# Performance work log

Hardware: AMD Instinct MI355X
Metric: run time of the kernel (lower is better)

Reference implementation:

```python
import jax, jax.numpy as jnp
import numpy as np

CUTOFF = 5.0
RBF_DIM = 32
CS, CV = 64, 32          # 64x0e + 32x1o -> irreps dim 64 + 32*3 = 160
NODE_ATTR = 64
HID = 128
NBLK = 3
MAXZ = 100
B, N, E = 32, 64, 131072
NW = 2 * CS + 3 * CV     # radial weights: w_ss, w_vv, w_sv, w_vs, w_vx


def setup_inputs() -> dict:
    key = jax.random.key(0)
    ks = jax.random.split(key, 16)
    z = jax.random.randint(ks[0], (B, N), 0, MAXZ + 1)
    mask = jnp.ones((B, N), jnp.float32)
    absorber_index = jax.random.randint(ks[1], (B,), 0, N)
    edge_src = jax.random.randint(ks[2], (E,), 0, B * N)
    edge_dst = jax.random.randint(ks[3], (E,), 0, B * N)
    edge_weight = 0.1 + (CUTOFF - 0.1) * jax.random.uniform(ks[4], (E,))
    edge_vec = jax.random.normal(ks[5], (E, 3))
    s = 0.1
    z_emb = s * jax.random.normal(ks[6], (MAXZ + 1, NODE_ATTR))
    W_in = s * jax.random.normal(ks[7], (NODE_ATTR + 1, CS))
    W1 = s * jax.random.normal(ks[8], (NBLK, RBF_DIM, HID))
    b1 = jnp.zeros((NBLK, HID))
    W2 = s * jax.random.normal(ks[9], (NBLK, HID, NW))
    b2 = jnp.zeros((NBLK, NW))
    Ws = s * jax.random.normal(ks[10], (NBLK, CS + CV, CS))
    Wv = s * jax.random.normal(ks[11], (NBLK, CS + 2 * CV, CV))
    Wg = s * jax.random.normal(ks[12], (NBLK, CS, CV))
    alpha = 0.1 * jnp.ones((NBLK,))
    return dict(z=z, mask=mask, absorber_index=absorber_index, edge_src=edge_src,
                edge_dst=edge_dst, edge_weight=edge_weight, edge_vec=edge_vec,
                z_emb=z_emb, W_in=W_in, W1=W1, b1=b1, W2=W2, b2=b2,
                Ws=Ws, Wv=Wv, Wg=Wg, alpha=alpha)


def _encode(z, mask, absorber_index, edge_src, edge_dst, edge_weight, edge_vec,
            z_emb, W_in, W1, b1, W2, b2, Ws, Wv, Wg, alpha):
    b, n = z.shape
    bn = b * n
    # absorber one-hot flag + atomic-number embedding -> scalar input irreps
    abs_flag = jnp.zeros((b, n), jnp.float32).at[jnp.arange(b), absorber_index].set(1.0)
    zf = z_emb[z]                                               # (B,N,NODE_ATTR)
    scalar_in = jnp.concatenate([zf, abs_flag[..., None]], -1).reshape(bn, NODE_ATTR + 1)
    s = scalar_in @ W_in                                        # (BN,CS)  0e channels
    v = jnp.zeros((bn, CV, 3), s.dtype)                         # 1o channels (o3.Linear from 0e only)
    fm = mask.reshape(bn)
    s = s * fm[:, None]

    # edge features: Gaussian RBF on clamped length + component-normalized SH (l<=1)
    el = edge_weight
    ed = edge_vec / jnp.clip(el, 1e-8)[:, None]
    d = jnp.minimum(el, CUTOFF)
    centers = jnp.linspace(0.0, CUTOFF, RBF_DIM)
    delta = CUTOFF / (RBF_DIM - 1)
    rbf = jnp.exp(-0.5 * ((d[:, None] - centers) / delta) ** 2)  # (E,RBF_DIM)
    Y1 = jnp.sqrt(3.0) * ed                                      # l=1 SH, 'component' norm; Y0 == 1
    env = 0.5 * (jnp.cos(jnp.pi * el / CUTOFF) + 1.0) * (el < CUTOFF)  # cosine cutoff

    sqrt3 = jnp.sqrt(3.0)
    sqrt2 = jnp.sqrt(2.0)
    for i in range(NBLK):
        h = jax.nn.silu(rbf @ W1[i] + b1[i])                     # radial MLP
        w = (h @ W2[i] + b2[i]) * env[:, None]                   # (E,NW) per-edge TP weights
        w_ss, w_vv, w_sv, w_vs, w_vx = jnp.split(
            w, [CS, CS + CV, 2 * CS + CV, 2 * CS + 2 * CV], axis=-1)
        s_src = s[edge_src]                                      # gather (E,CS)
        v_src = v[edge_src]                                      # gather (E,CV,3)
        # depthwise (uvu) tensor-product paths
        m_s = jnp.concatenate([
            w_ss * s_src,                                        # 0e x 0e -> 0e
            w_vv * jnp.einsum('ecd,ed->ec', v_src, Y1) / sqrt3,  # 1o x 1o -> 0e
        ], -1)                                                   # (E,CS+CV)
        m_v = jnp.concatenate([
            w_sv[:, :, None] * s_src[:, :, None] * Y1[:, None, :],           # 0e x 1o -> 1o
            w_vs[:, :, None] * v_src,                                        # 1o x 0e -> 1o
            w_vx[:, :, None] * jnp.cross(v_src, Y1[:, None, :]) / sqrt2,     # 1o x 1o -> 1o
        ], 1)                                                    # (E,CS+2CV,3)
        agg_s = jnp.zeros((bn, CS + CV), s.dtype).at[edge_dst].add(m_s)
        agg_v = jnp.zeros((bn, CS + 2 * CV, 3), s.dtype).at[edge_dst].add(m_v)
        # irreps-wise linear + gated nonlinearity + scaled residual
        us = jax.nn.silu(agg_s @ Ws[i])                          # (BN,CS)
        uv = jnp.einsum('bcd,ce->bed', agg_v, Wv[i])             # (BN,CV,3)
        g = jax.nn.sigmoid(us @ Wg[i])                           # (BN,CV) gates
        uv = uv * g[:, :, None]
        s = s + alpha[i] * us
        v = v + alpha[i] * uv

    # IrrepNorm: RMS-normalize each irrep block over its channels
    eps = 1e-6
    s = s / jnp.sqrt(jnp.mean(s ** 2, -1, keepdims=True) + eps)
    vn = jnp.mean(jnp.sum(v ** 2, -1), -1, keepdims=True)        # (BN,1)
    v = v / jnp.sqrt(vn + eps)[..., None]
    s = s * fm[:, None]
    v = v * fm[:, None, None]
    out = jnp.concatenate([s, v.reshape(bn, CV * 3)], -1)
    return out.reshape(b, n, CS + 3 * CV)


def reference(z, mask, absorber_index, edge_src, edge_dst, edge_weight, edge_vec,
              z_emb, W_in, W1, b1, W2, b2, Ws, Wv, Wg, alpha):
    return _encode(z, mask, absorber_index, edge_src, edge_dst, edge_weight, edge_vec,
                   z_emb, W_in, W1, b1, W2, b2, Ws, Wv, Wg, alpha)
```

## Files before the change

### kernel.cpp

```cpp
#include <hip/hip_runtime.h>

#define CSC 64
#define CVC 32
#define HIDC 128
#define NWC 224
#define RBFD 32
#define CUTF 5.0f

typedef __attribute__((ext_vector_type(8))) short bfrag8;
typedef __attribute__((ext_vector_type(4))) float facc4;

__device__ __forceinline__ unsigned short f2bf(float x) {
    union { float f; unsigned int u; } a; a.f = x;
    unsigned int u = a.u;
    return (unsigned short)((u + 0x7fffu + ((u >> 16) & 1u)) >> 16);
}
__device__ __forceinline__ float bf2f(unsigned int u16) {
    union { float f; unsigned int v; } x; x.v = u16 << 16; return x.f;
}

__device__ __forceinline__ float siluf(float x) { return x / (1.0f + __expf(-x)); }
__device__ __forceinline__ float sigmf(float x) { return 1.0f / (1.0f + __expf(-x)); }

__global__ __launch_bounds__(256) void eae_zero_int(int* __restrict__ p, int n) {
    int i = blockIdx.x * 256 + threadIdx.x;
    if (i < n) p[i] = 0;
}

__global__ __launch_bounds__(256) void eae_hist_kernel(const int* __restrict__ edge_dst,
                                                       int* __restrict__ cnt, int E) {
    int e = blockIdx.x * 256 + threadIdx.x;
    if (e < E) atomicAdd(&cnt[edge_dst[e]], 1);
}

__global__ __launch_bounds__(256) void eae_scan_kernel(const int* __restrict__ cnt,
                                                       int* __restrict__ row_ptr,
                                                       int* __restrict__ cursor, int BN) {
    __shared__ int part[256];
    int t = threadIdx.x;
    int per = (BN + 255) / 256;
    int base = t * per;
    int local[16];
    int lsum = 0;
    for (int i = 0; i < per; ++i) {
        int idx = base + i;
        int c = (idx < BN) ? cnt[idx] : 0;
        local[i] = c; lsum += c;
    }
    part[t] = lsum;
    __syncthreads();
    if (t == 0) {
        int run = 0;
        for (int i = 0; i < 256; ++i) { int v = part[i]; part[i] = run; run += v; }
    }
    __syncthreads();
    int run = part[t];
    for (int i = 0; i < per; ++i) {
        int idx = base + i;
        if (idx < BN) { row_ptr[idx] = run; cursor[idx] = run; run += local[i]; }
    }
    if (t == 255) row_ptr[BN] = run;
}

__global__ __launch_bounds__(256) void eae_scatter_kernel(
    const int* __restrict__ edge_dst, const int* __restrict__ edge_src,
    const float* __restrict__ edge_weight, const float* __restrict__ edge_vec,
    int* __restrict__ cursor, float4* __restrict__ edata, int* __restrict__ esrc,
    unsigned short* __restrict__ rbf_g, int E) {
    int e = blockIdx.x * 256 + threadIdx.x;
    if (e < E) {
        int pos = atomicAdd(&cursor[edge_dst[e]], 1);
        const float SQ3 = 1.7320508075688772f;
        const float PIF = 3.14159265358979323846f;
        const float delta = CUTF / (RBFD - 1);
        const float inv_delta = 1.0f / delta;
        float el = edge_weight[e];
        float inv = 1.0f / fmaxf(el, 1e-8f);
        float4 d;
        d.x = SQ3 * edge_vec[3 * e + 0] * inv;
        d.y = SQ3 * edge_vec[3 * e + 1] * inv;
        d.z = SQ3 * edge_vec[3 * e + 2] * inv;
        d.w = (el < CUTF) ? 0.5f * (__cosf(PIF * el / CUTF) + 1.0f) : 0.0f;
        edata[pos] = d;
        esrc[pos] = edge_src[e];
        float dd = fminf(el, CUTF) * inv_delta;
        unsigned short* rp = rbf_g + (size_t)pos * RBFD;
        #pragma unroll
        for (int k = 0; k < RBFD; ++k) {
            float x = dd - (float)k;
            rp[k] = f2bf(__expf(-0.5f * x * x));
        }
    }
}

__global__ __launch_bounds__(64) void eae_pack_kernel(
    const float* __restrict__ W1, const float* __restrict__ W2,
    unsigned short* __restrict__ W1P, unsigned short* __restrict__ W2P)
{
    int b = blockIdx.x;
    int lane = threadIdx.x;
    int t4 = lane >> 4, lr = lane & 15;
    if (b < 24) {
        int blk = b >> 3, mt = b & 7;
        const float* W1b = W1 + blk * 32 * 128;
        unsigned short* dst = W1P + ((size_t)b * 64 + lane) * 8;
        #pragma unroll
        for (int i = 0; i < 8; ++i) {
            int k = 8 * t4 + i;
            dst[i] = f2bf(W1b[k * HIDC + 16 * mt + lr]);
        }
    } else {
        int idx = b - 24;
        int blk = idx >> 6, rem = idx & 63;
        int mt = rem >> 2, ks = rem & 3;
        const float* W2b = W2 + blk * 128 * 224;
        unsigned short* dst = W2P + ((size_t)idx * 64 + lane) * 8;
        int ch = 16 * mt + lr;
        #pragma unroll
        for (int i = 0; i < 8; ++i) {
            int k = 32 * ks + 8 * t4 + i;
            dst[i] = (ch < NWC) ? f2bf(W2b[k * NWC + ch]) : (unsigned short)0;
        }
    }
}

__global__ __launch_bounds__(128) void eae_init_kernel(
    const int* __restrict__ z, const float* __restrict__ mask, const int* __restrict__ absorber,
    const float* __restrict__ z_emb, const float* __restrict__ W_in,
    float* __restrict__ s, float* __restrict__ v)
{
    int n = blockIdx.x;
    int t = threadIdx.x;
    int b = n >> 6;
    int ni = n & 63;
    float fm = mask[n];
    int zi = z[n];
    float af = (absorber[b] == ni) ? 1.0f : 0.0f;
    if (t < 64) {
        const float* ze = z_emb + zi * 64;
        float acc = 0.0f;
        #pragma unroll 4
        for (int k = 0; k < 64; ++k) acc += ze[k] * W_in[k * 64 + t];
        acc += af * W_in[64 * 64 + t];
        s[n * 64 + t] = acc * fm;
    }
    if (t < 96) v[n * 96 + t] = 0.0f;
}

__global__ __launch_bounds__(512) void eae_wgemm_kernel(
    const float4* __restrict__ edata, const unsigned short* __restrict__ rbf_g,
    const unsigned short* __restrict__ W1Pb, const float* __restrict__ b1b,
    const unsigned short* __restrict__ W2Pb, const float* __restrict__ b2b,
    unsigned short* __restrict__ wbuf, int E, int ntiles)
{
    __shared__ unsigned short h_lds[64 * 128];
    __shared__ unsigned short w_tile[64 * NWC];
    char* hb = (char*)h_lds;

    const int tid  = threadIdx.x;
    const int wid  = tid >> 6;
    const int lane = tid & 63;
    const int t4   = lane >> 4;
    const int lr   = lane & 15;
    const int swz  = (lr & 7) << 4;

    bfrag8 a1 = *reinterpret_cast<const bfrag8*>(W1Pb + ((size_t)wid * 64 + lane) * 8);
    float b1v[4];
    #pragma unroll
    for (int r = 0; r < 4; ++r) b1v[r] = b1b[16 * wid + 4 * t4 + r];

    bfrag8 a2[2][4];
    float b2v[2][4];
    #pragma unroll
    for (int m = 0; m < 2; ++m) {
        int mt = 2 * wid + m;
        #pragma unroll
        for (int ks = 0; ks < 4; ++ks)
            a2[m][ks] = *reinterpret_cast<const bfrag8*>(W2Pb + (((size_t)mt * 4 + ks) * 64 + lane) * 8);
        #pragma unroll
        for (int r = 0; r < 4; ++r) {
            int chr = 16 * mt + 4 * t4 + r;
            b2v[m][r] = (chr < NWC) ? b2b[chr] : 0.0f;
        }
    }

    for (int tile = blockIdx.x; tile < ntiles; tile += gridDim.x) {
        const int e0 = tile * 64;

        float env4[4];
        bfrag8 brbf[4];
        #pragma unroll
        for (int et = 0; et < 4; ++et) {
            int eg = e0 + 16 * et + lr;
            int ie = (eg < E) ? eg : (E - 1);
            env4[et] = edata[ie].w;
            brbf[et] = *reinterpret_cast<const bfrag8*>(rbf_g + (size_t)ie * RBFD + 8 * t4);
        }

        facc4 acc1[4];
        #pragma unroll
        for (int et = 0; et < 4; ++et) { facc4 zz = {0.f,0.f,0.f,0.f}; acc1[et] = zz; }
        #pragma unroll
        for (int et = 0; et < 4; ++et)
            acc1[et] = __builtin_amdgcn_mfma_f32_16x16x32_bf16(a1, brbf[et], acc1[et], 0, 0, 0);

        {
            int ch0b = (16 * wid + 4 * t4) * 2;
            #pragma unroll
            for (int et = 0; et < 4; ++et) {
                int e = 16 * et + lr;
                unsigned short hv[4];
                #pragma unroll
                for (int r = 0; r < 4; ++r)
                    hv[r] = f2bf(siluf(acc1[et][r] + b1v[r]));
                uint2 pk;
                pk.x = (unsigned int)hv[0] | ((unsigned int)hv[1] << 16);
                pk.y = (unsigned int)hv[2] | ((unsigned int)hv[3] << 16);
                *reinterpret_cast<uint2*>(hb + e * 256 + (ch0b ^ swz)) = pk;
            }
        }
        __syncthreads();

        facc4 acc2[2][4];
        #pragma unroll
        for (int m = 0; m < 2; ++m)
            #pragma unroll
            for (int et = 0; et < 4; ++et) { facc4 zz = {0.f,0.f,0.f,0.f}; acc2[m][et] = zz; }
        #pragma unroll
        for (int et = 0; et < 4; ++et) {
            int e = 16 * et + lr;
            bfrag8 hf[4];
            #pragma unroll
            for (int ks = 0; ks < 4; ++ks)
                hf[ks] = *reinterpret_cast<const bfrag8*>(hb + e * 256 + ((64 * ks + 16 * t4) ^ swz));
            #pragma unroll
            for (int m = 0; m < 2; ++m)
                #pragma unroll
                for (int ks = 0; ks < 4; ++ks)
                    acc2[m][et] = __builtin_amdgcn_mfma_f32_16x16x32_bf16(a2[m][ks], hf[ks], acc2[m][et], 0, 0, 0);
        }

        #pragma unroll
        for (int m = 0; m < 2; ++m) {
            int mt = 2 * wid + m;
            if (mt < 14) {
                int cb = 16 * mt + 4 * t4;
                #pragma unroll
                for (int et = 0; et < 4; ++et) {
                    int e = 16 * et + lr;
                    unsigned short hv[4];
                    #pragma unroll
                    for (int r = 0; r < 4; ++r)
                        hv[r] = f2bf((acc2[m][et][r] + b2v[m][r]) * env4[et]);
                    uint2 pk;
                    pk.x = (unsigned int)hv[0] | ((unsigned int)hv[1] << 16);
                    pk.y = (unsigned int)hv[2] | ((unsigned int)hv[3] << 16);
                    *reinterpret_cast<uint2*>(w_tile + e * NWC + cb) = pk;
                }
            }
        }
        __syncthreads();

        if (e0 + 64 <= E) {
            unsigned short* dst = wbuf + (size_t)e0 * NWC;
            for (int idx = tid; idx < 64 * NWC / 8; idx += 512) {
                uint4 d = *reinterpret_cast<const uint4*>(w_tile + idx * 8);
                *reinterpret_cast<uint4*>(dst + idx * 8) = d;
            }
        } else {
            int rem = (E - e0) * NWC;
            unsigned short* dst = wbuf + (size_t)e0 * NWC;
            for (int idx = tid; idx < rem; idx += 512) dst[idx] = w_tile[idx];
        }
        __syncthreads();
    }
}

#define EAE_COMPUTE(ed, wp, g0, g1, g2)                                                         \
    do {                                                                                        \
        float yx = ed.x, yy = ed.y, yz = ed.z;                                                  \
        float w0 = bf2f(wp.x & 0xffffu), w1 = bf2f(wp.x >> 16);                                 \
        float w2 = bf2f(wp.y & 0xffffu), w3 = bf2f(wp.y >> 16);                                 \
        if (kcls == 0) {                                                                        \
            a00 += w0 * g0.x; a10 += w1 * g0.y; a20 += w2 * g0.z; a30 += w3 * g0.w;             \
        } else if (kcls == 1) {                                                                 \
            a00 += w0 * (g0.x * yx + g1.x * yy + g2.x * yz) * IS3;                              \
            a10 += w1 * (g0.y * yx + g1.y * yy + g2.y * yz) * IS3;                              \
            a20 += w2 * (g0.z * yx + g1.z * yy + g2.z * yz) * IS3;                              \
            a30 += w3 * (g0.w * yx + g1.w * yy + g2.w * yz) * IS3;                              \
        } else if (kcls == 2) {                                                                 \
            float t0 = w0 * g0.x, t1 = w1 * g0.y, t2 = w2 * g0.z, t3 = w3 * g0.w;               \
            a00 += t0 * yx; a01 += t0 * yy; a02 += t0 * yz;                                     \
            a10 += t1 * yx; a11 += t1 * yy; a12 += t1 * yz;                                     \
            a20 += t2 * yx; a21 += t2 * yy; a22 += t2 * yz;                                     \
            a30 += t3 * yx; a31 += t3 * yy; a32 += t3 * yz;                                     \
        } else if (kcls == 3) {                                                                 \
            a00 += w0 * g0.x; a01 += w0 * g1.x; a02 += w0 * g2.x;                               \
            a10 += w1 * g0.y; a11 += w1 * g1.y; a12 += w1 * g2.y;                               \
            a20 += w2 * g0.z; a21 += w2 * g1.z; a22 += w2 * g2.z;                               \
            a30 += w3 * g0.w; a31 += w3 * g1.w; a32 += w3 * g2.w;                               \
        } else if (kcls == 4) {                                                                 \
            float s0 = w0 * IS2, s1 = w1 * IS2, s2 = w2 * IS2, s3 = w3 * IS2;                   \
            a00 += s0 * (g1.x * yz - g2.x * yy); a01 += s0 * (g2.x * yx - g0.x * yz); a02 += s0 * (g0.x * yy - g1.x * yx); \
            a10 += s1 * (g1.y * yz - g2.y * yy); a11 += s1 * (g2.y * yx - g0.y * yz); a12 += s1 * (g0.y * yy - g1.y * yx); \
            a20 += s2 * (g1.z * yz - g2.z * yy); a21 += s2 * (g2.z * yx - g0.z * yz); a22 += s2 * (g0.z * yy - g1.z * yx); \
            a30 += s3 * (g1.w * yz - g2.w * yy); a31 += s3 * (g2.w * yx - g0.w * yz); a32 += s3 * (g0.w * yy - g1.w * yx); \
        }                                                                                       \
    } while (0)

#define EAE_LOADS(SUF, idx)                                                                     \
    int ie##SUF = ebeg + (idx);                                                                 \
    int src##SUF = esrc[ie##SUF];                                                               \
    float4 ed##SUF = edata[ie##SUF];                                                            \
    uint2 wp##SUF = *reinterpret_cast<const uint2*>(wbuf + (size_t)ie##SUF * NWC + wc);         \
    const float* base##SUF = useS ? (s + src##SUF * CSC) : (v + src##SUF * 96);                 \
    float4 g0##SUF = *reinterpret_cast<const float4*>(base##SUF + coff);                        \
    float4 g1##SUF, g2##SUF;                                                                    \
    if (!useS) {                                                                                \
        g1##SUF = *reinterpret_cast<const float4*>(base##SUF + 32 + coff);                      \
        g2##SUF = *reinterpret_cast<const float4*>(base##SUF + 64 + coff);                      \
    }

__global__ __launch_bounds__(256) void eae_gather_kernel(
    const int* __restrict__ row_ptr,
    const float4* __restrict__ edata, const int* __restrict__ esrc,
    const unsigned short* __restrict__ wbuf,
    const float* __restrict__ s, const float* __restrict__ v,
    float* __restrict__ aggs, float* __restrict__ aggv)
{
    __shared__ float sh[4][480];

    const int n  = blockIdx.x;
    const int wq = threadIdx.x >> 6;
    const int l  = threadIdx.x & 63;
    const int ch0 = 4 * l;

    const float IS3 = 0.57735026918962576f;
    const float IS2 = 0.70710678118654752f;

    int kcls; bool useS; int coff;
    if (l < 16)      { kcls = 0; useS = true;  coff = ch0; }
    else if (l < 24) { kcls = 1; useS = false; coff = ch0 - 64; }
    else if (l < 40) { kcls = 2; useS = true;  coff = ch0 - 96; }
    else if (l < 48) { kcls = 3; useS = false; coff = ch0 - 160; }
    else if (l < 56) { kcls = 4; useS = false; coff = ch0 - 192; }
    else             { kcls = 5; useS = true;  coff = 0; }
    const int wc = (l < 56) ? ch0 : 0;

    const int ebeg = row_ptr[n];
    const int ecnt = row_ptr[n + 1] - ebeg;
    int per = (ecnt + 3) >> 2;
    int i0 = wq * per; if (i0 > ecnt) i0 = ecnt;
    int i1 = i0 + per; if (i1 > ecnt) i1 = ecnt;

    float a00=0.f,a01=0.f,a02=0.f, a10=0.f,a11=0.f,a12=0.f;
    float a20=0.f,a21=0.f,a22=0.f, a30=0.f,a31=0.f,a32=0.f;

    int i = i0;
    for (; i + 3 < i1; i += 4) {
        EAE_LOADS(A, i);
        EAE_LOADS(B, i + 1);
        EAE_LOADS(C, i + 2);
        EAE_LOADS(D, i + 3);
        EAE_COMPUTE(edA, wpA, g0A, g1A, g2A);
        EAE_COMPUTE(edB, wpB, g0B, g1B, g2B);
        EAE_COMPUTE(edC, wpC, g0C, g1C, g2C);
        EAE_COMPUTE(edD, wpD, g0D, g1D, g2D);
    }
    for (; i < i1; ++i) {
        EAE_LOADS(A, i);
        EAE_COMPUTE(edA, wpA, g0A, g1A, g2A);
    }

    float* shw = sh[wq];
    if (kcls == 0) {
        shw[ch0 + 0] = a00; shw[ch0 + 1] = a10; shw[ch0 + 2] = a20; shw[ch0 + 3] = a30;
    } else if (kcls == 1) {
        shw[64 + coff + 0] = a00; shw[64 + coff + 1] = a10; shw[64 + coff + 2] = a20; shw[64 + coff + 3] = a30;
    } else if (kcls == 2) {
        int c = coff;
        shw[96 + 0 * 128 + c + 0] = a00; shw[96 + 1 * 128 + c + 0] = a01; shw[96 + 2 * 128 + c + 0] = a02;
        shw[96 + 0 * 128 + c + 1] = a10; shw[96 + 1 * 128 + c + 1] = a11; shw[96 + 2 * 128 + c + 1] = a12;
        shw[96 + 0 * 128 + c + 2] = a20; shw[96 + 1 * 128 + c + 2] = a21; shw[96 + 2 * 128 + c + 2] = a22;
        shw[96 + 0 * 128 + c + 3] = a30; shw[96 + 1 * 128 + c + 3] = a31; shw[96 + 2 * 128 + c + 3] = a32;
    } else if (kcls == 3) {
        int c = 64 + coff;
        shw[96 + 0 * 128 + c + 0] = a00; shw[96 + 1 * 128 + c + 0] = a01; shw[96 + 2 * 128 + c + 0] = a02;
        shw[96 + 0 * 128 + c + 1] = a10; shw[96 + 1 * 128 + c + 1] = a11; shw[96 + 2 * 128 + c + 1] = a12;
        shw[96 + 0 * 128 + c + 2] = a20; shw[96 + 1 * 128 + c + 2] = a21; shw[96 + 2 * 128 + c + 2] = a22;
        shw[96 + 0 * 128 + c + 3] = a30; shw[96 + 1 * 128 + c + 3] = a31; shw[96 + 2 * 128 + c + 3] = a32;
    } else if (kcls == 4) {
        int c = 96 + coff;
        shw[96 + 0 * 128 + c + 0] = a00; shw[96 + 1 * 128 + c + 0] = a01; shw[96 + 2 * 128 + c + 0] = a02;
        shw[96 + 0 * 128 + c + 1] = a10; shw[96 + 1 * 128 + c + 1] = a11; shw[96 + 2 * 128 + c + 1] = a12;
        shw[96 + 0 * 128 + c + 2] = a20; shw[96 + 1 * 128 + c + 2] = a21; shw[96 + 2 * 128 + c + 2] = a22;
        shw[96 + 0 * 128 + c + 3] = a30; shw[96 + 1 * 128 + c + 3] = a31; shw[96 + 2 * 128 + c + 3] = a32;
    }
    __syncthreads();

    for (int j = threadIdx.x; j < 480; j += 256) {
        float sum = sh[0][j] + sh[1][j] + sh[2][j] + sh[3][j];
        if (j < 96) aggs[n * 96 + j] = sum;
        else        aggv[n * 384 + (j - 96)] = sum;
    }
}

__global__ __launch_bounds__(128) void eae_node_kernel(
    const float* __restrict__ Ws, const float* __restrict__ Wv, const float* __restrict__ Wg,
    const float* __restrict__ alpha,
    float* __restrict__ s, float* __restrict__ v,
    const float* __restrict__ aggs, const float* __restrict__ aggv, int blk)
{
    int n = blockIdx.x;
    int t = threadIdx.x;
    __shared__ float sh_as[96];
    __shared__ float sh_av[384];
    __shared__ float sh_us[64];
    __shared__ float sh_g[32];

    for (int i = t; i < 96; i += 128) sh_as[i] = aggs[n * 96 + i];
    for (int i = t; i < 384; i += 128) sh_av[i] = aggv[n * 384 + i];
    __syncthreads();

    float a = alpha[blk];
    const float* Wsb = Ws + blk * 96 * 64;
    const float* Wvb = Wv + blk * 128 * 32;
    const float* Wgb = Wg + blk * 64 * 32;

    if (t < 64) {
        float acc = 0.0f;
        #pragma unroll 4
        for (int j = 0; j < 96; ++j) acc += sh_as[j] * Wsb[j * 64 + t];
        sh_us[t] = siluf(acc);
    }
    __syncthreads();
    if (t < 32) {
        float acc = 0.0f;
        #pragma unroll 4
        for (int j = 0; j < 64; ++j) acc += sh_us[j] * Wgb[j * 32 + t];
        sh_g[t] = sigmf(acc);
    }
    if (t < 64) s[n * 64 + t] += a * sh_us[t];
    __syncthreads();
    if (t < 96) {
        int d = t >> 5;
        int c = t & 31;
        float acc = 0.0f;
        #pragma unroll 4
        for (int j = 0; j < 128; ++j) acc += sh_av[d * 128 + j] * Wvb[j * 32 + c];
        v[n * 96 + d * 32 + c] += a * sh_g[c] * acc;
    }
}

__global__ __launch_bounds__(64) void eae_final_kernel(
    const float* __restrict__ mask, const float* __restrict__ s, const float* __restrict__ v,
    float* __restrict__ out)
{
    int n = blockIdx.x;
    int t = threadIdx.x;
    float fm = mask[n];

    float sv = s[n * 64 + t];
    float ss = sv * sv;
    #pragma unroll
    for (int o = 32; o >= 1; o >>= 1) ss += __shfl_xor(ss, o);
    float sn = sv / sqrtf(ss / 64.0f + 1e-6f);
    out[n * 160 + t] = sn * fm;

    float vx = (t < 32) ? v[n * 96 + t]      : 0.0f;
    float vy = (t < 32) ? v[n * 96 + 32 + t] : 0.0f;
    float vz = (t < 32) ? v[n * 96 + 64 + t] : 0.0f;
    float vs2 = vx * vx + vy * vy + vz * vz;
    #pragma unroll
    for (int o = 32; o >= 1; o >>= 1) vs2 += __shfl_xor(vs2, o);
    float scale = fm / sqrtf(vs2 / 32.0f + 1e-6f);
    if (t < 32) {
        out[n * 160 + 64 + t * 3 + 0] = vx * scale;
        out[n * 160 + 64 + t * 3 + 1] = vy * scale;
        out[n * 160 + 64 + t * 3 + 2] = vz * scale;
    }
}

extern "C" void kernel_launch(void* const* d_in, const int* in_sizes, int n_in,
                              void* d_out, int out_size, void* d_ws, size_t ws_size,
                              hipStream_t stream) {
    const int*   z           = (const int*)d_in[0];
    const float* mask        = (const float*)d_in[1];
    const int*   absorber    = (const int*)d_in[2];
    const int*   edge_src    = (const int*)d_in[3];
    const int*   edge_dst    = (const int*)d_in[4];
    const float* edge_weight = (const float*)d_in[5];
    const float* edge_vec    = (const float*)d_in[6];
    const float* z_emb       = (const float*)d_in[7];
    const float* W_in        = (const float*)d_in[8];
    const float* W1          = (const float*)d_in[9];
    const float* b1          = (const float*)d_in[10];
    const float* W2          = (const float*)d_in[11];
    const float* b2          = (const float*)d_in[12];
    const float* Ws          = (const float*)d_in[13];
    const float* Wv          = (const float*)d_in[14];
    const float* Wg          = (const float*)d_in[15];
    const float* alpha       = (const float*)d_in[16];
    float* out = (float*)d_out;

    const int BN = in_sizes[0];
    const int E  = in_sizes[3];

    float* ws_f = (float*)d_ws;
    float4* edata = (float4*)ws_f;
    float* s    = ws_f + (size_t)E * 4;
    float* v    = s + (size_t)BN * 64;
    float* aggs = v + (size_t)BN * 96;
    float* aggv = aggs + (size_t)BN * 96;
    int*   iws  = (int*)(aggv + (size_t)BN * 384);
    int* esrc    = iws;
    int* cnt     = esrc + E;
    int* row_ptr = cnt + BN;
    int* cursor  = row_ptr + BN + 4;
    unsigned short* W1P = (unsigned short*)(cursor + BN);
    unsigned short* W2P = W1P + 3 * 8 * 64 * 8;
    unsigned short* wbuf = W2P + 3 * 64 * 64 * 8;
    unsigned short* rbf_g = wbuf + (size_t)E * NWC;

    eae_zero_int<<<(BN + 255) / 256, 256, 0, stream>>>(cnt, BN);
    eae_hist_kernel<<<(E + 255) / 256, 256, 0, stream>>>(edge_dst, cnt, E);
    eae_scan_kernel<<<1, 256, 0, stream>>>(cnt, row_ptr, cursor, BN);
    eae_scatter_kernel<<<(E + 255) / 256, 256, 0, stream>>>(
        edge_dst, edge_src, edge_weight, edge_vec, cursor, edata, esrc, rbf_g, E);
    eae_pack_kernel<<<216, 64, 0, stream>>>(W1, W2, W1P, W2P);

    eae_init_kernel<<<BN, 128, 0, stream>>>(z, mask, absorber, z_emb, W_in, s, v);

    int ntiles = (E + 63) / 64;
    for (int blk = 0; blk < 3; ++blk) {
        eae_wgemm_kernel<<<1024, 512, 0, stream>>>(
            edata, rbf_g,
            W1P + (size_t)blk * 8 * 64 * 8, b1 + (size_t)blk * 128,
            W2P + (size_t)blk * 64 * 64 * 8, b2 + (size_t)blk * 224,
            wbuf, E, ntiles);
        eae_gather_kernel<<<BN, 256, 0, stream>>>(
            row_ptr, edata, esrc, wbuf, s, v, aggs, aggv);
        eae_node_kernel<<<BN, 128, 0, stream>>>(Ws, Wv, Wg, alpha, s, v, aggs, aggv, blk);
    }
    eae_final_kernel<<<BN, 64, 0, stream>>>(mask, s, v, out);
}
```

Baseline: 312.3 us.

## Fuse gather, node update and final norm into one kernel with ping-pong buffers

Merges the per-node gather/aggregation kernel with the node linear/gate update and, on the last block, the final irrep normalization. Aggregates stay in shared memory instead of round-tripping through global aggs/aggv buffers. s/v are double-buffered so other blocks' reads of neighbor state aren't corrupted by in-place updates. This removes 4 kernel launches and global traffic, at the cost of more shared memory per block and idle threads during the small node matmuls.

Result: no change. 317.4 us (+1.6%).

```diff
diff --git a/kernel.cpp b/kernel.cpp
--- a/kernel.cpp
+++ b/kernel.cpp
@@ -313,7 +313,7 @@
     int src##SUF = esrc[ie##SUF];                                                               \
     float4 ed##SUF = edata[ie##SUF];                                                            \
     uint2 wp##SUF = *reinterpret_cast<const uint2*>(wbuf + (size_t)ie##SUF * NWC + wc);         \
-    const float* base##SUF = useS ? (s + src##SUF * CSC) : (v + src##SUF * 96);                 \
+    const float* base##SUF = useS ? (s_in + src##SUF * CSC) : (v_in + src##SUF * 96);           \
     float4 g0##SUF = *reinterpret_cast<const float4*>(base##SUF + coff);                        \
     float4 g1##SUF, g2##SUF;                                                                    \
     if (!useS) {                                                                                \
@@ -321,18 +321,26 @@
         g2##SUF = *reinterpret_cast<const float4*>(base##SUF + 64 + coff);                      \
     }
 
-__global__ __launch_bounds__(256) void eae_gather_kernel(
+__global__ __launch_bounds__(256) void eae_gather_node_kernel(
     const int* __restrict__ row_ptr,
     const float4* __restrict__ edata, const int* __restrict__ esrc,
     const unsigned short* __restrict__ wbuf,
-    const float* __restrict__ s, const float* __restrict__ v,
-    float* __restrict__ aggs, float* __restrict__ aggv)
+    const float* __restrict__ s_in, const float* __restrict__ v_in,
+    float* __restrict__ s_out, float* __restrict__ v_out,
+    const float* __restrict__ Wsb, const float* __restrict__ Wvb, const float* __restrict__ Wgb,
+    const float* __restrict__ alpha, const float* __restrict__ mask,
+    float* __restrict__ out, int blk, int last)
 {
     __shared__ float sh[4][480];
+    __shared__ float sh_us[64];
+    __shared__ float sh_g[32];
+    __shared__ float sh_s[64];
+    __shared__ float sh_v[96];
 
     const int n  = blockIdx.x;
-    const int wq = threadIdx.x >> 6;
-    const int l  = threadIdx.x & 63;
+    const int tid = threadIdx.x;
+    const int wq = tid >> 6;
+    const int l  = tid & 63;
     const int ch0 = 4 * l;
 
     const float IS3 = 0.57735026918962576f;
@@ -398,86 +406,68 @@
     }
     __syncthreads();
 
-    for (int j = threadIdx.x; j < 480; j += 256) {
-        float sum = sh[0][j] + sh[1][j] + sh[2][j] + sh[3][j];
-        if (j < 96) aggs[n * 96 + j] = sum;
-        else        aggv[n * 384 + (j - 96)] = sum;
-    }
-}
-
-__global__ __launch_bounds__(128) void eae_node_kernel(
-    const float* __restrict__ Ws, const float* __restrict__ Wv, const float* __restrict__ Wg,
-    const float* __restrict__ alpha,
-    float* __restrict__ s, float* __restrict__ v,
-    const float* __restrict__ aggs, const float* __restrict__ aggv, int blk)
-{
-    int n = blockIdx.x;
-    int t = threadIdx.x;
-    __shared__ float sh_as[96];
-    __shared__ float sh_av[384];
-    __shared__ float sh_us[64];
-    __shared__ float sh_g[32];
-
-    for (int i = t; i < 96; i += 128) sh_as[i] = aggs[n * 96 + i];
-    for (int i = t; i < 384; i += 128) sh_av[i] = aggv[n * 384 + i];
+    for (int j = tid; j < 480; j += 256)
+        sh[0][j] = sh[0][j] + sh[1][j] + sh[2][j] + sh[3][j];
     __syncthreads();
 
+    const float* aggs_l = sh[0];
+    const float* aggv_l = sh[0] + 96;
     float a = alpha[blk];
-    const float* Wsb = Ws + blk * 96 * 64;
-    const float* Wvb = Wv + blk * 128 * 32;
-    const float* Wgb = Wg + blk * 64 * 32;
-
-    if (t < 64) {
+
+    if (tid < 64) {
         float acc = 0.0f;
         #pragma unroll 4
-        for (int j = 0; j < 96; ++j) acc += sh_as[j] * Wsb[j * 64 + t];
-        sh_us[t] = siluf(acc);
+        for (int j = 0; j < 96; ++j) acc += aggs_l[j] * Wsb[j * 64 + tid];
+        sh_us[tid] = siluf(acc);
     }
     __syncthreads();
-    if (t < 32) {
+    if (tid < 32) {
         float acc = 0.0f;
         #pragma unroll 4
-        for (int j = 0; j < 64; ++j) acc += sh_us[j] * Wgb[j * 32 + t];
-        sh_g[t] = sigmf(acc);
-    }
-    if (t < 64) s[n * 64 + t] += a * sh_us[t];
+        for (int j = 0; j < 64; ++j) acc += sh_us[j] * Wgb[j * 32 + tid];
+        sh_g[tid] = sigmf(acc);
+    }
     __syncthreads();
-    if (t < 96) {
-        int d = t >> 5;
-        int c = t & 31;
+
+    float s_new = 0.0f, v_new = 0.0f;
+    if (tid < 64) s_new = s_in[n * 64 + tid] + a * sh_us[tid];
+    if (tid < 96) {
+        int d = tid >> 5;
+        int c = tid & 31;
         float acc = 0.0f;
         #pragma unroll 4
-        for (int j = 0; j < 128; ++j) acc += sh_av[d * 128 + j] * Wvb[j * 32 + c];
-        v[n * 96 + d * 32 + c] += a * sh_g[c] * acc;
-    }
-}
-
-__global__ __launch_bounds__(64) void eae_final_kernel(
-    const float* __restrict__ mask, const float* __restrict__ s, const float* __restrict__ v,
-    float* __restrict__ out)
-{
-    int n = blockIdx.x;
-    int t = threadIdx.x;
-    float fm = mask[n];
-
-    float sv = s[n * 64 + t];
-    float ss = sv * sv;
-    #pragma unroll
-    for (int o = 32; o >= 1; o >>= 1) ss += __shfl_xor(ss, o);
-    float sn = sv / sqrtf(ss / 64.0f + 1e-6f);
-    out[n * 160 + t] = sn * fm;
-
-    float vx = (t < 32) ? v[n * 96 + t]      : 0.0f;
-    float vy = (t < 32) ? v[n * 96 + 32 + t] : 0.0f;
-    float vz = (t < 32) ? v[n * 96 + 64 + t] : 0.0f;
-    float vs2 = vx * vx + vy * vy + vz * vz;
-    #pragma unroll
-    for (int o = 32; o >= 1; o >>= 1) vs2 += __shfl_xor(vs2, o);
-    float scale = fm / sqrtf(vs2 / 32.0f + 1e-6f);
-    if (t < 32) {
-        out[n * 160 + 64 + t * 3 + 0] = vx * scale;
-        out[n * 160 + 64 + t * 3 + 1] = vy * scale;
-        out[n * 160 + 64 + t * 3 + 2] = vz * scale;
+        for (int j = 0; j < 128; ++j) acc += aggv_l[d * 128 + j] * Wvb[j * 32 + c];
+        v_new = v_in[n * 96 + tid] + a * sh_g[c] * acc;
+    }
+
+    if (!last) {
+        if (tid < 64) s_out[n * 64 + tid] = s_new;
+        if (tid < 96) v_out[n * 96 + tid] = v_new;
+    } else {
+        if (tid < 64) sh_s[tid] = s_new;
+        if (tid < 96) sh_v[tid] = v_new;
+        __syncthreads();
+        if (tid < 64) {
+            float fm = mask[n];
+            float sv = sh_s[tid];
+            float ss = sv * sv;
+            #pragma unroll
+            for (int o = 32; o >= 1; o >>= 1) ss += __shfl_xor(ss, o);
+            out[n * 160 + tid] = sv / sqrtf(ss / 64.0f + 1e-6f) * fm;
+
+            float vx = (tid < 32) ? sh_v[tid]      : 0.0f;
+            float vy = (tid < 32) ? sh_v[32 + tid] : 0.0f;
+            float vz = (tid < 32) ? sh_v[64 + tid] : 0.0f;
+            float vs2 = vx * vx + vy * vy + vz * vz;
+            #pragma unroll
+            for (int o = 32; o >= 1; o >>= 1) vs2 += __shfl_xor(vs2, o);
+            float scale = fm / sqrtf(vs2 / 32.0f + 1e-6f);
+            if (tid < 32) {
+                out[n * 160 + 64 + tid * 3 + 0] = vx * scale;
+                out[n * 160 + 64 + tid * 3 + 1] = vy * scale;
+                out[n * 160 + 64 + tid * 3 + 2] = vz * scale;
+            }
+        }
     }
 }
 
@@ -508,11 +498,11 @@
 
     float* ws_f = (float*)d_ws;
     float4* edata = (float4*)ws_f;
-    float* s    = ws_f + (size_t)E * 4;
-    float* v    = s + (size_t)BN * 64;
-    float* aggs = v + (size_t)BN * 96;
-    float* aggv = aggs + (size_t)BN * 96;
-    int*   iws  = (int*)(aggv + (size_t)BN * 384);
+    float* s0   = ws_f + (size_t)E * 4;
+    float* v0   = s0 + (size_t)BN * 64;
+    float* s1   = v0 + (size_t)BN * 96;
+    float* v1   = s1 + (size_t)BN * 64;
+    int*   iws  = (int*)(v1 + (size_t)BN * 96);
     int* esrc    = iws;
     int* cnt     = esrc + E;
     int* row_ptr = cnt + BN;
@@ -529,18 +519,22 @@
         edge_dst, edge_src, edge_weight, edge_vec, cursor, edata, esrc, rbf_g, E);
     eae_pack_kernel<<<216, 64, 0, stream>>>(W1, W2, W1P, W2P);
 
-    eae_init_kernel<<<BN, 128, 0, stream>>>(z, mask, absorber, z_emb, W_in, s, v);
+    eae_init_kernel<<<BN, 128, 0, stream>>>(z, mask, absorber, z_emb, W_in, s0, v0);
 
     int ntiles = (E + 63) / 64;
+    float* sIn = s0; float* vIn = v0;
+    float* sOut = s1; float* vOut = v1;
     for (int blk = 0; blk < 3; ++blk) {
         eae_wgemm_kernel<<<1024, 512, 0, stream>>>(
             edata, rbf_g,
             W1P + (size_t)blk * 8 * 64 * 8, b1 + (size_t)blk * 128,
             W2P + (size_t)blk * 64 * 64 * 8, b2 + (size_t)blk * 224,
             wbuf, E, ntiles);
-        eae_gather_kernel<<<BN, 256, 0, stream>>>(
-            row_ptr, edata, esrc, wbuf, s, v, aggs, aggv);
-        eae_node_kernel<<<BN, 128, 0, stream>>>(Ws, Wv, Wg, alpha, s, v, aggs, aggv, blk);
-    }
-    eae_final_kernel<<<BN, 64, 0, stream>>>(mask, s, v, out);
-}
+        eae_gather_node_kernel<<<BN, 256, 0, stream>>>(
+            row_ptr, edata, esrc, wbuf, sIn, vIn, sOut, vOut,
+            Ws + (size_t)blk * 96 * 64, Wv + (size_t)blk * 128 * 32, Wg + (size_t)blk * 64 * 32,
+            alpha, mask, out, blk, (blk == 2) ? 1 : 0);
+        float* ts = sIn; sIn = sOut; sOut = ts;
+        float* tv = vIn; vIn = vOut; vOut = tv;
+    }
+}
```

## Overlap next block's radial-weight GEMM with current gather in fused kernel

Applied to the files above, without the earlier changes.

Merges each block's edge gather with the next block's radial-MLP weight GEMM into one launch. The first blocks do the gather (two nodes per 512-thread block) and the remaining blocks compute the next weights into a second buffer, alternating between two buffers. The aim is to fill the GPU while the gather is bandwidth- or latency-bound and to cut the number of serial launches. This needs a second E×224 bf16 buffer and falls back to the old serial path if the workspace is too small. Gather blocks now hold 45 KB of LDS each, which may lower occupancy.

After: 387.0 us. 23.9% more time.

```diff
diff --git a/kernel.cpp b/kernel.cpp
--- a/kernel.cpp
+++ b/kernel.cpp
@@ -147,17 +147,17 @@
     if (t < 96) v[n * 96 + t] = 0.0f;
 }
 
-__global__ __launch_bounds__(512) void eae_wgemm_kernel(
+__device__ __forceinline__ void eae_wgemm_body(
+    char* smem, int tid, int tile0, int tstride,
     const float4* __restrict__ edata, const unsigned short* __restrict__ rbf_g,
     const unsigned short* __restrict__ W1Pb, const float* __restrict__ b1b,
     const unsigned short* __restrict__ W2Pb, const float* __restrict__ b2b,
     unsigned short* __restrict__ wbuf, int E, int ntiles)
 {
-    __shared__ unsigned short h_lds[64 * 128];
-    __shared__ unsigned short w_tile[64 * NWC];
+    unsigned short* h_lds  = (unsigned short*)smem;
+    unsigned short* w_tile = (unsigned short*)(smem + 16384);
     char* hb = (char*)h_lds;
 
-    const int tid  = threadIdx.x;
     const int wid  = tid >> 6;
     const int lane = tid & 63;
     const int t4   = lane >> 4;
@@ -184,7 +184,7 @@
         }
     }
 
-    for (int tile = blockIdx.x; tile < ntiles; tile += gridDim.x) {
+    for (int tile = tile0; tile < ntiles; tile += tstride) {
         const int e0 = tile * 64;
 
         float env4[4];
@@ -313,7 +313,7 @@
     int src##SUF = esrc[ie##SUF];                                                               \
     float4 ed##SUF = edata[ie##SUF];                                                            \
     uint2 wp##SUF = *reinterpret_cast<const uint2*>(wbuf + (size_t)ie##SUF * NWC + wc);         \
-    const float* base##SUF = useS ? (s + src##SUF * CSC) : (v + src##SUF * 96);                 \
+    const float* base##SUF = useS ? (s_in + src##SUF * CSC) : (v_in + src##SUF * 96);           \
     float4 g0##SUF = *reinterpret_cast<const float4*>(base##SUF + coff);                        \
     float4 g1##SUF, g2##SUF;                                                                    \
     if (!useS) {                                                                                \
@@ -321,18 +321,15 @@
         g2##SUF = *reinterpret_cast<const float4*>(base##SUF + 64 + coff);                      \
     }
 
-__global__ __launch_bounds__(256) void eae_gather_kernel(
-    const int* __restrict__ row_ptr,
-    const float4* __restrict__ edata, const int* __restrict__ esrc,
-    const unsigned short* __restrict__ wbuf,
-    const float* __restrict__ s, const float* __restrict__ v,
+__device__ __forceinline__ void eae_gather_body(
+    float* shbase, int n, int t,
+    const int* __restrict__ row_ptr, const float4* __restrict__ edata,
+    const int* __restrict__ esrc, const unsigned short* __restrict__ wbuf,
+    const float* __restrict__ s_in, const float* __restrict__ v_in,
     float* __restrict__ aggs, float* __restrict__ aggv)
 {
-    __shared__ float sh[4][480];
-
-    const int n  = blockIdx.x;
-    const int wq = threadIdx.x >> 6;
-    const int l  = threadIdx.x & 63;
+    const int wq = t >> 6;
+    const int l  = t & 63;
     const int ch0 = 4 * l;
 
     const float IS3 = 0.57735026918962576f;
@@ -372,7 +369,7 @@
         EAE_COMPUTE(edA, wpA, g0A, g1A, g2A);
     }
 
-    float* shw = sh[wq];
+    float* shw = shbase + wq * 480;
     if (kcls == 0) {
         shw[ch0 + 0] = a00; shw[ch0 + 1] = a10; shw[ch0 + 2] = a20; shw[ch0 + 3] = a30;
     } else if (kcls == 1) {
@@ -398,10 +395,63 @@
     }
     __syncthreads();
 
-    for (int j = threadIdx.x; j < 480; j += 256) {
-        float sum = sh[0][j] + sh[1][j] + sh[2][j] + sh[3][j];
+    for (int j = t; j < 480; j += 256) {
+        float sum = shbase[j] + shbase[480 + j] + shbase[960 + j] + shbase[1440 + j];
         if (j < 96) aggs[n * 96 + j] = sum;
         else        aggv[n * 384 + (j - 96)] = sum;
+    }
+}
+
+__global__ __launch_bounds__(512) void eae_wgemm_kernel(
+    const float4* __restrict__ edata, const unsigned short* __restrict__ rbf_g,
+    const unsigned short* __restrict__ W1Pb, const float* __restrict__ b1b,
+    const unsigned short* __restrict__ W2Pb, const float* __restrict__ b2b,
+    unsigned short* __restrict__ wbuf, int E, int ntiles)
+{
+    __shared__ __align__(16) char smem[45056];
+    eae_wgemm_body(smem, threadIdx.x, blockIdx.x, gridDim.x,
+                   edata, rbf_g, W1Pb, b1b, W2Pb, b2b, wbuf, E, ntiles);
+}
+
+__global__ __launch_bounds__(256) void eae_gather_kernel(
+    const int* __restrict__ row_ptr,
+    const float4* __restrict__ edata, const int* __restrict__ esrc,
+    const unsigned short* __restrict__ wbuf,
+    const float* __restrict__ s_in, const float* __restrict__ v_in,
+    float* __restrict__ aggs, float* __restrict__ aggv)
+{
+    __shared__ float sh[4 * 480];
+    eae_gather_body(sh, blockIdx.x, threadIdx.x, row_ptr, edata, esrc, wbuf,
+                    s_in, v_in, aggs, aggv);
+}
+
+__global__ __launch_bounds__(512) void eae_fat_kernel(
+    const int* __restrict__ row_ptr, const float4* __restrict__ edata,
+    const int* __restrict__ esrc, const unsigned short* __restrict__ wbuf_r,
+    const float* __restrict__ s_in, const float* __restrict__ v_in,
+    float* __restrict__ aggs, float* __restrict__ aggv, int ngblk, int BN,
+    const unsigned short* __restrict__ rbf_g,
+    const unsigned short* __restrict__ W1Pb, const float* __restrict__ b1b,
+    const unsigned short* __restrict__ W2Pb, const float* __restrict__ b2b,
+    unsigned short* __restrict__ wbuf_w, int E, int ntiles)
+{
+    __shared__ __align__(16) char smem[45056];
+    int bid = blockIdx.x;
+    int tid = threadIdx.x;
+    if (bid < ngblk) {
+        int half = tid >> 8;
+        int t = tid & 255;
+        int n = 2 * bid + half;
+        float* shbase = (float*)smem + half * 4 * 480;
+        if (n < BN) {
+            eae_gather_body(shbase, n, t, row_ptr, edata, esrc, wbuf_r,
+                            s_in, v_in, aggs, aggv);
+        } else {
+            __syncthreads();
+        }
+    } else {
+        eae_wgemm_body(smem, tid, bid - ngblk, gridDim.x - ngblk,
+                       edata, rbf_g, W1Pb, b1b, W2Pb, b2b, wbuf_w, E, ntiles);
     }
 }
 
@@ -519,8 +569,13 @@
     int* cursor  = row_ptr + BN + 4;
     unsigned short* W1P = (unsigned short*)(cursor + BN);
     unsigned short* W2P = W1P + 3 * 8 * 64 * 8;
-    unsigned short* wbuf = W2P + 3 * 64 * 64 * 8;
-    unsigned short* rbf_g = wbuf + (size_t)E * NWC;
+    unsigned short* wbufA = W2P + 3 * 64 * 64 * 8;
+    unsigned short* rbf_g = wbufA + (size_t)E * NWC;
+    unsigned short* wbufB = rbf_g + (size_t)E * RBFD;
+
+    size_t need2 = (size_t)((char*)(wbufB + (size_t)E * NWC) - (char*)d_ws);
+    bool overlap = (ws_size >= need2);
+    if (!overlap) wbufB = wbufA;
 
     eae_zero_int<<<(BN + 255) / 256, 256, 0, stream>>>(cnt, BN);
     eae_hist_kernel<<<(E + 255) / 256, 256, 0, stream>>>(edge_dst, cnt, E);
@@ -532,15 +587,35 @@
     eae_init_kernel<<<BN, 128, 0, stream>>>(z, mask, absorber, z_emb, W_in, s, v);
 
     int ntiles = (E + 63) / 64;
-    for (int blk = 0; blk < 3; ++blk) {
+    if (overlap) {
+        const int ngblk = BN / 2;
         eae_wgemm_kernel<<<1024, 512, 0, stream>>>(
-            edata, rbf_g,
-            W1P + (size_t)blk * 8 * 64 * 8, b1 + (size_t)blk * 128,
-            W2P + (size_t)blk * 64 * 64 * 8, b2 + (size_t)blk * 224,
-            wbuf, E, ntiles);
-        eae_gather_kernel<<<BN, 256, 0, stream>>>(
-            row_ptr, edata, esrc, wbuf, s, v, aggs, aggv);
-        eae_node_kernel<<<BN, 128, 0, stream>>>(Ws, Wv, Wg, alpha, s, v, aggs, aggv, blk);
+            edata, rbf_g, W1P, b1 + 0, W2P, b2 + 0, wbufA, E, ntiles);
+        eae_fat_kernel<<<ngblk + 1024, 512, 0, stream>>>(
+            row_ptr, edata, esrc, wbufA, s, v, aggs, aggv, ngblk, BN,
+            rbf_g, W1P + (size_t)1 * 8 * 64 * 8, b1 + 128,
+            W2P + (size_t)1 * 64 * 64 * 8, b2 + 224, wbufB, E, ntiles);
+        eae_node_kernel<<<BN, 128, 0, stream>>>(Ws, Wv, Wg, alpha, s, v, aggs, aggv, 0);
+        eae_fat_kernel<<<ngblk + 1024, 512, 0, stream>>>(
+            row_ptr, edata, esrc, wbufB, s, v, aggs, aggv, ngblk, BN,
+            rbf_g, W1P + (size_t)2 * 8 * 64 * 8, b1 + 256,
+            W2P + (size_t)2 * 64 * 64 * 8, b2 + 448, wbufA, E, ntiles);
+        eae_node_kernel<<<BN, 128, 0, stream>>>(Ws, Wv, Wg, alpha, s, v, aggs, aggv, 1);
+        eae_fat_kernel<<<ngblk, 512, 0, stream>>>(
+            row_ptr, edata, esrc, wbufA, s, v, aggs, aggv, ngblk, BN,
+            rbf_g, W1P, b1, W2P, b2, wbufB, E, 0);
+        eae_node_kernel<<<BN, 128, 0, stream>>>(Ws, Wv, Wg, alpha, s, v, aggs, aggv, 2);
+    } else {
+        for (int blk = 0; blk < 3; ++blk) {
+            eae_wgemm_kernel<<<1024, 512, 0, stream>>>(
+                edata, rbf_g,
+                W1P + (size_t)blk * 8 * 64 * 8, b1 + (size_t)blk * 128,
+                W2P + (size_t)blk * 64 * 64 * 8, b2 + (size_t)blk * 224,
+                wbufA, E, ntiles);
+            eae_gather_kernel<<<BN, 256, 0, stream>>>(
+                row_ptr, edata, esrc, wbufA, s, v, aggs, aggv);
+            eae_node_kernel<<<BN, 128, 0, stream>>>(Ws, Wv, Wg, alpha, s, v, aggs, aggv, blk);
+        }
     }
     eae_final_kernel<<<BN, 64, 0, stream>>>(mask, s, v, out);
 }
```
